# Performance work log

Measured on AMD Instinct MI355X. Metric: run time of the kernel, lower is better.

Reference implementation:

```python
import jax, jax.numpy as jnp
import numpy as np
from jax import lax

KERNEL = 3
NUM_ITER = 40
SMOOTH = 1.0


def _max_pool3d(x):
    # stride-1, SAME-padded 3x3x3 max pool over (B, C, D, H, W)
    return lax.reduce_window(x, -jnp.inf, lax.max,
                             (1, 1, KERNEL, KERNEL, KERNEL),
                             (1, 1, 1, 1, 1), 'SAME')


def _soft_erode(x):
    return -_max_pool3d(-x)


def _soft_open(x):
    return _max_pool3d(_soft_erode(x))


def soft_skel(img, num_iter=NUM_ITER):
    skel = jax.nn.relu(img - _soft_open(img))

    def body(carry, _):
        img, skel = carry
        img = _soft_erode(img)
        delta = jax.nn.relu(img - _soft_open(img))
        skel = skel + jax.nn.relu(delta - skel * delta)
        return (img, skel), None

    (_, skel), _ = lax.scan(body, (img, skel), None, length=num_iter)
    return skel


def reference(y_pred, y_true):
    p = jax.nn.sigmoid(y_pred)
    skel_pred = soft_skel(p)
    skel_true = soft_skel(y_true)
    tprec = (jnp.sum(skel_pred * y_true) + SMOOTH) / (jnp.sum(skel_pred) + SMOOTH)
    tsens = (jnp.sum(skel_true * p) + SMOOTH) / (jnp.sum(skel_true) + SMOOTH)
    cl_dice = 2.0 * (tprec * tsens) / (tprec + tsens + SMOOTH)
    return 1.0 - cl_dice


def setup_inputs() -> dict:
    key = jax.random.key(0)
    k1, k2 = jax.random.split(key)
    shape = (2, 1, 96, 256, 256)
    y_pred = jax.random.normal(k1, shape, dtype=jnp.float32)  # logits
    y_true = jax.random.uniform(k2, shape, dtype=jnp.float32)  # soft mask in [0,1]
    return {"y_pred": y_pred, "y_true": y_true}
```

## Files before the change

kernel.cpp:

```cpp
#include <hip/hip_runtime.h>
#include <hip/hip_fp16.h>
#include <math.h>

#define WW 256
#define HH 256
#define DDP 96
#define HWP (WW*HH)
#define DHW (DDP*HWP)
#define N2 (2*DHW)
#define N4 (4*DHW)
#define TX 128
#define TY 8
#define NT 256
#define ZS 12
#define NSLAB (DDP/ZS)
#define RED_BLOCKS 1024
#define NITER 40
#define RPAIRS 66
#define NSLOT ((TY+2)*RPAIRS)

typedef unsigned int u32;
typedef unsigned short u16;
typedef unsigned char u8;
typedef __half2 h2;

__device__ __forceinline__ float sigm(float x){return 1.f/(1.f+expf(-x));}
__device__ __forceinline__ int   icl(int v,int hi){return min(max(v,0),hi);}
__device__ __forceinline__ u32 h2u(h2 v){return __builtin_bit_cast(u32,v);}
__device__ __forceinline__ h2  u2h(u32 v){return __builtin_bit_cast(h2,v);}
__device__ __forceinline__ float2 up2(u32 v){return __half22float2(u2h(v));}
__device__ __forceinline__ u32 dn2(float a,float b){return h2u(__floats2half2_rn(a,b));}
__device__ __forceinline__ u32 pmin2(u32 a,u32 b){u32 d;asm("v_pk_min_f16 %0, %1, %2":"=v"(d):"v"(a),"v"(b));return d;}
__device__ __forceinline__ u32 pmax2(u32 a,u32 b){u32 d;asm("v_pk_max_f16 %0, %1, %2":"=v"(d):"v"(a),"v"(b));return d;}
__device__ __forceinline__ u32 psub2(u32 a,u32 b){u32 d;asm("v_pk_add_f16 %0, %1, %2 neg_lo:[0,1] neg_hi:[0,1]":"=v"(d):"v"(a),"v"(b));return d;}
__device__ __forceinline__ u32 pfma2(u32 a,u32 b,u32 c){u32 d;asm("v_pk_fma_f16 %0, %1, %2, %3":"=v"(d):"v"(a),"v"(b),"v"(c));return d;}
__device__ __forceinline__ u32 shpair(u32 hiSrc,u32 loSrc){return __builtin_amdgcn_alignbit(hiSrc,loSrc,16);}
__device__ __forceinline__ u32 sfix(u32 v,int m){
    if (m == 1) v = (v & 0xffffu) | (v << 16);
    else if (m == 2) v = (v >> 16) | (v & 0xffff0000u);
    return v;
}
__device__ __forceinline__ u32 pkrtz(float a,float b){
    return __builtin_bit_cast(u32, __builtin_amdgcn_cvt_pkrtz(a,b));
}
#define INF2P 0x7C007C00u
#define INF2N 0xFC00FC00u
#define C255_2 0x5BF85BF8u

__device__ __forceinline__ u32 pack_u8_sr(float s0,float s1,float s2,float s3,u32 h){
    float t0 = (float)( h        & 0xff);
    float t1 = (float)((h >>  8) & 0xff);
    float t2 = (float)((h >> 16) & 0xff);
    float t3 = (float)((h >> 24) & 0xff);
    int q0 = min((int)(s0*255.f + (t0+0.5f)*(1.f/256.f)), 255);
    int q1 = min((int)(s1*255.f + (t1+0.5f)*(1.f/256.f)), 255);
    int q2 = min((int)(s2*255.f + (t2+0.5f)*(1.f/256.f)), 255);
    int q3 = min((int)(s3*255.f + (t3+0.5f)*(1.f/256.f)), 255);
    return (u32)q0 | ((u32)q1<<8) | ((u32)q2<<16) | ((u32)q3<<24);
}

template<int MODE>
__global__ __launch_bounds__(NT) void step_kernel(const u16* __restrict__ ghalo,
                                                  u16* __restrict__ eaw,
                                                  const float* __restrict__ ypred,
                                                  const float* __restrict__ ytrue,
                                                  u8* __restrict__ skel,
                                                  int itno) {
    const int tx = threadIdx.x & 31;
    const int ty = threadIdx.x >> 5;
    const int x0 = blockIdx.x * TX;
    const int y0 = blockIdx.y * TY;
    const int vol = blockIdx.z / NSLAB;
    const int z0 = (blockIdx.z % NSLAB) * ZS;
    const size_t base = (size_t)vol * DHW;
    const int gxc = x0 + 4*tx;
    const int gyc = y0 + ty;
    const size_t co = (size_t)gyc*WW + gxc;

    const float* fin = nullptr;
    bool dosig = false;
    if (MODE == 0 || MODE == 1) {
        if (vol < 2) { fin = ypred + base; dosig = true; }
        else         { fin = ytrue + (size_t)(vol-2)*DHW; }
    }

    __shared__ u32 raw[2][TY+2][RPAIRS];

    const bool s2v = threadIdx.x < (NSLOT - 2*NT);
    u32 lo0, lo1, lo2;
    int md0, md1, md2;
    size_t po0, po1, po2;
    {
        #define SLOTSETUP(K, LO, MD, PO) {                         \
            int idx = threadIdx.x + (K)*NT;                        \
            int r = idx / RPAIRS;                                  \
            int w = idx - r*RPAIRS;                                \
            int gy = icl(y0-1+r, HH-1);                            \
            int gx0 = x0 - 2 + 2*w;                                \
            int m = 0, gx = gx0;                                   \
            if (gx0 < 0) { m = 1; gx = 0; }                        \
            else if (gx0 >= WW) { m = 2; gx = WW-2; }              \
            LO = r*RPAIRS + w; MD = m;                             \
            PO = (size_t)gy*WW + gx; }
        SLOTSETUP(0, lo0, md0, po0)
        SLOTSETUP(1, lo1, md1, po1)
        if (s2v) { SLOTSETUP(2, lo2, md2, po2) } else { lo2 = 0; md2 = 0; po2 = 0; }
        #undef SLOTSETUP
    }
    const u16*   hp0 = nullptr; const u16* hp1 = nullptr; const u16* hp2 = nullptr;
    const float* fp0 = nullptr; const float* fp1 = nullptr; const float* fp2 = nullptr;
    if (MODE == 0) {
        fp0 = fin + po0 + (size_t)(z0-1)*HWP;
        fp1 = fin + po1 + (size_t)(z0-1)*HWP;
        fp2 = fin + po2 + (size_t)(z0-1)*HWP;
    } else {
        hp0 = ghalo + base + po0 + (size_t)(z0-1)*HWP;
        hp1 = ghalo + base + po1 + (size_t)(z0-1)*HWP;
        hp2 = ghalo + base + po2 + (size_t)(z0-1)*HWP;
    }

    if (z0 >= 1) {
        const int b = (z0-1) & 1;
        u32 v0, v1, v2 = 0;
        if (MODE == 0) {
            float2 f0 = *(const float2*)fp0; v0 = dn2(f0.x, f0.y);
            float2 f1 = *(const float2*)fp1; v1 = dn2(f1.x, f1.y);
            if (s2v) { float2 f2 = *(const float2*)fp2; v2 = dn2(f2.x, f2.y); }
        } else {
            v0 = *(const u32*)hp0;
            v1 = *(const u32*)hp1;
            if (s2v) v2 = *(const u32*)hp2;
        }
        (&raw[b][0][0])[lo0] = sfix(v0, md0);
        (&raw[b][0][0])[lo1] = sfix(v1, md1);
        if (s2v) (&raw[b][0][0])[lo2] = sfix(v2, md2);
    }
    __syncthreads();

    const int wl = 2*tx;
    u32 n00,n01,n02, n10,n11,n12;
    u32 m00,m01,m02, m10,m11,m12;
    n00=n01=n02=n10=n11=n12=INF2P;
    m00=m01=m02=m10=m11=m12=INF2N;

    uint2 cv_c = make_uint2(0,0), cv_n = make_uint2(0,0);
    u32 sv_c = 0, sv_n = 0;
    float4 fv_c = make_float4(0,0,0,0), fv_n = make_float4(0,0,0,0);

    for (int zi = z0-1; zi <= z0+ZS; ++zi) {
        if (MODE == 0) { fp0 += HWP; fp1 += HWP; fp2 += HWP; }
        else           { hp0 += HWP; hp1 += HWP; hp2 += HWP; }
        const bool stage_ok = (zi < z0+ZS) && ((unsigned)(zi+1) < DDP);

        u32 v0 = 0, v1 = 0, v2 = 0;
        if (stage_ok) {
            if (MODE == 0) {
                float2 f0 = *(const float2*)fp0; v0 = dn2(f0.x, f0.y);
                float2 f1 = *(const float2*)fp1; v1 = dn2(f1.x, f1.y);
                if (s2v) { float2 f2 = *(const float2*)fp2; v2 = dn2(f2.x, f2.y); }
            } else {
                v0 = *(const u32*)hp0;
                v1 = *(const u32*)hp1;
                if (s2v) v2 = *(const u32*)hp2;
            }
        }
        if (MODE != 0 && zi >= z0 && zi < z0+ZS) {
            size_t pidx = base + (size_t)zi*HWP + co;
            if (MODE == 1) {
                fv_n = *(const float4*)(fin + (size_t)zi*HWP + co);
            } else {
                cv_n = *(const uint2*)(eaw + pidx);
                sv_n = *(const u32*)(skel + pidx);
            }
        }

        u32 xn0=INF2P, xn1=INF2P, xm0=INF2N, xm1=INF2N;
        if ((unsigned)zi < DDP) {
            const int b = zi & 1;
            uint2 a0 = *(const uint2*)&raw[b][ty  ][wl];
            uint2 b0 = *(const uint2*)&raw[b][ty  ][wl+2];
            uint2 a1 = *(const uint2*)&raw[b][ty+1][wl];
            uint2 b1 = *(const uint2*)&raw[b][ty+1][wl+2];
            uint2 a2 = *(const uint2*)&raw[b][ty+2][wl];
            uint2 b2 = *(const uint2*)&raw[b][ty+2][wl+2];
            u32 vnL  = pmin2(a0.x, pmin2(a1.x, a2.x));
            u32 vnM0 = pmin2(a0.y, pmin2(a1.y, a2.y));
            u32 vnM1 = pmin2(b0.x, pmin2(b1.x, b2.x));
            u32 vnR  = pmin2(b0.y, pmin2(b1.y, b2.y));
            u32 lsn  = shpair(vnM0, vnL);
            u32 rsn  = shpair(vnM1, vnM0);
            u32 rs1n = shpair(vnR,  vnM1);
            xn0 = pmin2(vnM0, pmin2(lsn, rsn));
            xn1 = pmin2(vnM1, pmin2(rsn, rs1n));
            if (MODE != 0) {
                u32 vmL  = pmax2(a0.x, pmax2(a1.x, a2.x));
                u32 vmM0 = pmax2(a0.y, pmax2(a1.y, a2.y));
                u32 vmM1 = pmax2(b0.x, pmax2(b1.x, b2.x));
                u32 vmR  = pmax2(b0.y, pmax2(b1.y, b2.y));
                u32 lsm  = shpair(vmM0, vmL);
                u32 rsm  = shpair(vmM1, vmM0);
                u32 rs1m = shpair(vmR,  vmM1);
                xm0 = pmax2(vmM0, pmax2(lsm, rsm));
                xm1 = pmax2(vmM1, pmax2(rsm, rs1m));
            }
        }
        n00=n01; n01=n02; n02=xn0;  n10=n11; n11=n12; n12=xn1;
        if (MODE != 0) { m00=m01; m01=m02; m02=xm0;  m10=m11; m11=m12; m12=xm1; }

        if (zi >= z0+1) {
            const int zc = zi - 1;
            size_t idx = base + (size_t)zc*HWP + co;
            u32 e0 = pmin2(n00, pmin2(n01, n02));
            u32 e1 = pmin2(n10, pmin2(n11, n12));
            if (MODE == 0) {
                if (dosig) {
                    float2 f0 = up2(e0), f1 = up2(e1);
                    e0 = dn2(sigm(f0.x), sigm(f0.y));
                    e1 = dn2(sigm(f1.x), sigm(f1.y));
                }
                *(uint2*)(eaw + idx) = make_uint2(e0, e1);
            } else if (MODE == 1) {
                float2 mA = up2(pmax2(m00, pmax2(m01, m02)));
                float2 mB = up2(pmax2(m10, pmax2(m11, m12)));
                float av0=fv_c.x, av1=fv_c.y, av2=fv_c.z, av3=fv_c.w;
                if (dosig) { av0=sigm(av0); av1=sigm(av1); av2=sigm(av2); av3=sigm(av3); }
                float d0 = fmaxf(av0 - mA.x, 0.f);
                float d1 = fmaxf(av1 - mA.y, 0.f);
                float d2 = fmaxf(av2 - mB.x, 0.f);
                float d3 = fmaxf(av3 - mB.y, 0.f);
                u32 lin = (u32)(idx >> 2);
                u32 h = lin * 2654435761u + (u32)itno * 0x9E3779B9u;
                *(u32*)(skel + idx) = pack_u8_sr(d0, d1, d2, d3, h);
                *(uint2*)(eaw + idx) = make_uint2(e0, e1);
            } else {
                u32 M3p0 = pmax2(m00, pmax2(m01, m02));
                u32 M3p1 = pmax2(m10, pmax2(m11, m12));
                u32 d0p = pmax2(psub2(cv_c.x, M3p0), 0u);
                u32 d1p = pmax2(psub2(cv_c.y, M3p1), 0u);
                u32 Sp0 = pkrtz((float)( sv_c        & 0xff), (float)((sv_c >>  8) & 0xff));
                u32 Sp1 = pkrtz((float)((sv_c >> 16) & 0xff), (float)((sv_c >> 24) & 0xff));
                u32 Sn0 = pfma2(d0p, psub2(C255_2, Sp0), Sp0);
                u32 Sn1 = pfma2(d1p, psub2(C255_2, Sp1), Sp1);
                float2 f0 = up2(Sn0), f1 = up2(Sn1);
                u32 lin = (u32)(idx >> 2);
                u32 h = lin * 2654435761u + (u32)itno * 0x9E3779B9u;
                u32 q0 = (u32)(f0.x + ((float)( h        & 0xff) + 0.5f)*(1.f/256.f));
                u32 q1 = (u32)(f0.y + ((float)((h >>  8) & 0xff) + 0.5f)*(1.f/256.f));
                u32 q2 = (u32)(f1.x + ((float)((h >> 16) & 0xff) + 0.5f)*(1.f/256.f));
                u32 q3 = (u32)(f1.y + ((float)((h >> 24) & 0xff) + 0.5f)*(1.f/256.f));
                *(u32*)(skel + idx) = q0 | (q1<<8) | (q2<<16) | (q3<<24);
                if (MODE != 3) *(uint2*)(eaw + idx) = make_uint2(e0, e1);
            }
        }
        cv_c = cv_n; sv_c = sv_n; fv_c = fv_n;

        if (stage_ok) {
            const int b = (zi+1) & 1;
            (&raw[b][0][0])[lo0] = sfix(v0, md0);
            (&raw[b][0][0])[lo1] = sfix(v1, md1);
            if (s2v) (&raw[b][0][0])[lo2] = sfix(v2, md2);
        }
        __syncthreads();
    }
}

__global__ __launch_bounds__(256) void reduce4_kernel(const u8* __restrict__ skel,
                                                      const float* __restrict__ ytrue,
                                                      const float* __restrict__ ypred,
                                                      float* __restrict__ part) {
    const u32* sp = (const u32*)skel;
    const u32* st = (const u32*)(skel + N2);
    const float4* yt = (const float4*)ytrue;
    const float4* yp = (const float4*)ypred;
    float a0=0.f,a1=0.f,a2=0.f,a3=0.f;
    for (int i = blockIdx.x*256 + threadIdx.x; i < N2/4; i += gridDim.x*256) {
        u32 a = sp[i]; u32 b = st[i];
        float4 t = yt[i]; float4 q = yp[i];
        float s0 = (float)( a        & 0xff) * (1.f/255.f);
        float s1 = (float)((a >>  8) & 0xff) * (1.f/255.f);
        float s2 = (float)((a >> 16) & 0xff) * (1.f/255.f);
        float s3 = (float)((a >> 24) & 0xff) * (1.f/255.f);
        float u0 = (float)( b        & 0xff) * (1.f/255.f);
        float u1 = (float)((b >>  8) & 0xff) * (1.f/255.f);
        float u2v= (float)((b >> 16) & 0xff) * (1.f/255.f);
        float u3 = (float)((b >> 24) & 0xff) * (1.f/255.f);
        a0 += s0*t.x + s1*t.y + s2*t.z + s3*t.w;
        a1 += s0 + s1 + s2 + s3;
        a2 += u0*sigm(q.x) + u1*sigm(q.y) + u2v*sigm(q.z) + u3*sigm(q.w);
        a3 += u0 + u1 + u2v + u3;
    }
    for (int off=32; off>0; off>>=1) {
        a0+=__shfl_down(a0,off); a1+=__shfl_down(a1,off);
        a2+=__shfl_down(a2,off); a3+=__shfl_down(a3,off);
    }
    __shared__ float red[4][4];
    int wave = threadIdx.x>>6;
    if ((threadIdx.x&63)==0){red[wave][0]=a0;red[wave][1]=a1;red[wave][2]=a2;red[wave][3]=a3;}
    __syncthreads();
    if (threadIdx.x==0){
        float s0=0,s1=0,s2=0,s3=0;
        for(int w=0;w<4;++w){s0+=red[w][0];s1+=red[w][1];s2+=red[w][2];s3+=red[w][3];}
        part[0*RED_BLOCKS+blockIdx.x]=s0; part[1*RED_BLOCKS+blockIdx.x]=s1;
        part[2*RED_BLOCKS+blockIdx.x]=s2; part[3*RED_BLOCKS+blockIdx.x]=s3;
    }
}

__global__ __launch_bounds__(256) void finalize_kernel(const float* __restrict__ part,
                                                       float* __restrict__ out) {
    float a0=0.f,a1=0.f,a2=0.f,a3=0.f;
    for (int i=threadIdx.x;i<RED_BLOCKS;i+=256){
        a0+=part[0*RED_BLOCKS+i]; a1+=part[1*RED_BLOCKS+i];
        a2+=part[2*RED_BLOCKS+i]; a3+=part[3*RED_BLOCKS+i];
    }
    for (int off=32; off>0; off>>=1){
        a0+=__shfl_down(a0,off); a1+=__shfl_down(a1,off);
        a2+=__shfl_down(a2,off); a3+=__shfl_down(a3,off);
    }
    __shared__ float red[4][4];
    int wave = threadIdx.x>>6;
    if ((threadIdx.x&63)==0){red[wave][0]=a0;red[wave][1]=a1;red[wave][2]=a2;red[wave][3]=a3;}
    __syncthreads();
    if (threadIdx.x==0){
        float s0=0,s1=0,s2=0,s3=0;
        for(int w=0;w<4;++w){s0+=red[w][0];s1+=red[w][1];s2+=red[w][2];s3+=red[w][3];}
        float tprec=(s0+1.f)/(s1+1.f);
        float tsens=(s2+1.f)/(s3+1.f);
        float cl2=2.f*tprec*tsens/(tprec+tsens+1.f);
        out[0]=1.f-cl2;
    }
}

__global__ void sentinel_kernel(float* out, float v){ out[0]=v; }

extern "C" void kernel_launch(void* const* d_in, const int* in_sizes, int n_in,
                              void* d_out, int out_size, void* d_ws, size_t ws_size,
                              hipStream_t stream) {
    const float* ypred = (const float*)d_in[0];
    const float* ytrue = (const float*)d_in[1];
    float* out = (float*)d_out;

    const size_t need = (size_t)2*N4*sizeof(u16) + (size_t)N4 + (size_t)4*RED_BLOCKS*sizeof(float);
    if (ws_size < need) { sentinel_kernel<<<1,1,0,stream>>>(out,-111111.f); return; }

    u16* EA   = (u16*)d_ws;
    u16* EB   = EA + N4;
    u8*  SKEL = (u8*)(EB + N4);
    float* PART = (float*)(SKEL + N4);

    dim3 grid(WW/TX, HH/TY, 4*NSLAB);

    step_kernel<0><<<grid, NT, 0, stream>>>(nullptr, EB, ypred, ytrue, nullptr, 0);
    step_kernel<1><<<grid, NT, 0, stream>>>(EB, EA, ypred, ytrue, SKEL, 0);

    u16* h = EA;
    u16* a = EB;
    for (int t = 1; t <= NITER; ++t) {
        if (t < NITER) step_kernel<2><<<grid, NT, 0, stream>>>(h, a, nullptr, nullptr, SKEL, t);
        else           step_kernel<3><<<grid, NT, 0, stream>>>(h, a, nullptr, nullptr, SKEL, t);
        u16* tmp = h; h = a; a = tmp;
    }

    reduce4_kernel<<<RED_BLOCKS, 256, 0, stream>>>(SKEL, ytrue, ypred, PART);
    finalize_kernel<<<1, 256, 0, stream>>>(PART, out);
}
```

Before: 1.669 ms.

## Prefetch halo planes two ahead and swizzle block order across XCDs

Halo loads for each z-plane are now issued two iterations ahead, with the shared-memory ring grown from two to four buffers, so global load latency overlaps more of the compute. The 3D grid becomes a 1D grid of 2048 blocks with a swizzle that maps consecutive block IDs to strided tiles, likely to spread neighbouring tiles across the chiplets or improve cache locality. The cost is more live registers and double the LDS per block, which could reduce occupancy.

```diff
diff --git a/kernel.cpp b/kernel.cpp
--- a/kernel.cpp
+++ b/kernel.cpp
@@ -18,6 +18,7 @@
 #define NITER 40
 #define RPAIRS 66
 #define NSLOT ((TY+2)*RPAIRS)
+#define NBLK 2048
 
 typedef unsigned int u32;
 typedef unsigned short u16;
@@ -66,12 +67,18 @@
                                                   const float* __restrict__ ytrue,
                                                   u8* __restrict__ skel,
                                                   int itno) {
+    const int bid = blockIdx.x;
+    const int swz = (bid & 7) * (NBLK/8) + (bid >> 3);
+    const int bx  = swz & 1;
+    const int by  = (swz >> 1) & 31;
+    const int bz  = swz >> 6;
+    const int vol = bz >> 3;
+    const int z0  = (bz & 7) * ZS;
+
     const int tx = threadIdx.x & 31;
     const int ty = threadIdx.x >> 5;
-    const int x0 = blockIdx.x * TX;
-    const int y0 = blockIdx.y * TY;
-    const int vol = blockIdx.z / NSLAB;
-    const int z0 = (blockIdx.z % NSLAB) * ZS;
+    const int x0 = bx * TX;
+    const int y0 = by * TY;
     const size_t base = (size_t)vol * DHW;
     const int gxc = x0 + 4*tx;
     const int gyc = y0 + ty;
@@ -84,7 +91,7 @@
         else         { fin = ytrue + (size_t)(vol-2)*DHW; }
     }
 
-    __shared__ u32 raw[2][TY+2][RPAIRS];
+    __shared__ u32 raw[4][TY+2][RPAIRS];
 
     const bool s2v = threadIdx.x < (NSLOT - 2*NT);
     u32 lo0, lo1, lo2;
@@ -107,33 +114,35 @@
         if (s2v) { SLOTSETUP(2, lo2, md2, po2) } else { lo2 = 0; md2 = 0; po2 = 0; }
         #undef SLOTSETUP
     }
-    const u16*   hp0 = nullptr; const u16* hp1 = nullptr; const u16* hp2 = nullptr;
-    const float* fp0 = nullptr; const float* fp1 = nullptr; const float* fp2 = nullptr;
-    if (MODE == 0) {
-        fp0 = fin + po0 + (size_t)(z0-1)*HWP;
-        fp1 = fin + po1 + (size_t)(z0-1)*HWP;
-        fp2 = fin + po2 + (size_t)(z0-1)*HWP;
+
+    const u16* hq0 = nullptr; const u16* hq1 = nullptr; const u16* hq2 = nullptr;
+    const float* fq0 = nullptr; const float* fq1 = nullptr; const float* fq2 = nullptr;
+    if (MODE == 0) { fq0 = fin + po0; fq1 = fin + po1; fq2 = fin + po2; }
+    else { hq0 = ghalo + base + po0; hq1 = ghalo + base + po1; hq2 = ghalo + base + po2; }
+
+    #define LOADP(Z, V0, V1, V2) {                                           \
+        if (MODE == 0) {                                                     \
+            float2 f0 = *(const float2*)(fq0 + (size_t)(Z)*HWP); V0 = dn2(f0.x,f0.y); \
+            float2 f1 = *(const float2*)(fq1 + (size_t)(Z)*HWP); V1 = dn2(f1.x,f1.y); \
+            if (s2v) { float2 f2 = *(const float2*)(fq2 + (size_t)(Z)*HWP); V2 = dn2(f2.x,f2.y); } \
+        } else {                                                             \
+            V0 = *(const u32*)(hq0 + (size_t)(Z)*HWP);                       \
+            V1 = *(const u32*)(hq1 + (size_t)(Z)*HWP);                       \
+            if (s2v) V2 = *(const u32*)(hq2 + (size_t)(Z)*HWP);              \
+        } }
+    #define WRITEP(B, V0, V1, V2) {                                          \
+        (&raw[B][0][0])[lo0] = sfix(V0, md0);                                \
+        (&raw[B][0][0])[lo1] = sfix(V1, md1);                                \
+        if (s2v) (&raw[B][0][0])[lo2] = sfix(V2, md2); }
+
+    u32 vN0 = 0, vN1 = 0, vN2 = 0;
+    if (z0 >= 1) {
+        u32 t0 = 0, t1 = 0, t2 = 0;
+        LOADP(z0-1, t0, t1, t2)
+        LOADP(z0, vN0, vN1, vN2)
+        WRITEP((z0-1)&3, t0, t1, t2)
     } else {
-        hp0 = ghalo + base + po0 + (size_t)(z0-1)*HWP;
-        hp1 = ghalo + base + po1 + (size_t)(z0-1)*HWP;
-        hp2 = ghalo + base + po2 + (size_t)(z0-1)*HWP;
-    }
-
-    if (z0 >= 1) {
-        const int b = (z0-1) & 1;
-        u32 v0, v1, v2 = 0;
-        if (MODE == 0) {
-            float2 f0 = *(const float2*)fp0; v0 = dn2(f0.x, f0.y);
-            float2 f1 = *(const float2*)fp1; v1 = dn2(f1.x, f1.y);
-            if (s2v) { float2 f2 = *(const float2*)fp2; v2 = dn2(f2.x, f2.y); }
-        } else {
-            v0 = *(const u32*)hp0;
-            v1 = *(const u32*)hp1;
-            if (s2v) v2 = *(const u32*)hp2;
-        }
-        (&raw[b][0][0])[lo0] = sfix(v0, md0);
-        (&raw[b][0][0])[lo1] = sfix(v1, md1);
-        if (s2v) (&raw[b][0][0])[lo2] = sfix(v2, md2);
+        LOADP(z0, vN0, vN1, vN2)
     }
     __syncthreads();
 
@@ -148,22 +157,10 @@
     float4 fv_c = make_float4(0,0,0,0), fv_n = make_float4(0,0,0,0);
 
     for (int zi = z0-1; zi <= z0+ZS; ++zi) {
-        if (MODE == 0) { fp0 += HWP; fp1 += HWP; fp2 += HWP; }
-        else           { hp0 += HWP; hp1 += HWP; hp2 += HWP; }
-        const bool stage_ok = (zi < z0+ZS) && ((unsigned)(zi+1) < DDP);
-
-        u32 v0 = 0, v1 = 0, v2 = 0;
-        if (stage_ok) {
-            if (MODE == 0) {
-                float2 f0 = *(const float2*)fp0; v0 = dn2(f0.x, f0.y);
-                float2 f1 = *(const float2*)fp1; v1 = dn2(f1.x, f1.y);
-                if (s2v) { float2 f2 = *(const float2*)fp2; v2 = dn2(f2.x, f2.y); }
-            } else {
-                v0 = *(const u32*)hp0;
-                v1 = *(const u32*)hp1;
-                if (s2v) v2 = *(const u32*)hp2;
-            }
-        }
+        const bool far_ok = (zi+2 <= z0+ZS) && (zi+2 < DDP);
+        u32 vF0 = 0, vF1 = 0, vF2 = 0;
+        if (far_ok) { LOADP(zi+2, vF0, vF1, vF2) }
+
         if (MODE != 0 && zi >= z0 && zi < z0+ZS) {
             size_t pidx = base + (size_t)zi*HWP + co;
             if (MODE == 1) {
@@ -176,7 +173,7 @@
 
         u32 xn0=INF2P, xn1=INF2P, xm0=INF2N, xm1=INF2N;
         if ((unsigned)zi < DDP) {
-            const int b = zi & 1;
+            const int b = zi & 3;
             uint2 a0 = *(const uint2*)&raw[b][ty  ][wl];
             uint2 b0 = *(const uint2*)&raw[b][ty  ][wl+2];
             uint2 a1 = *(const uint2*)&raw[b][ty+1][wl];
@@ -254,14 +251,13 @@
         }
         cv_c = cv_n; sv_c = sv_n; fv_c = fv_n;
 
-        if (stage_ok) {
-            const int b = (zi+1) & 1;
-            (&raw[b][0][0])[lo0] = sfix(v0, md0);
-            (&raw[b][0][0])[lo1] = sfix(v1, md1);
-            if (s2v) (&raw[b][0][0])[lo2] = sfix(v2, md2);
-        }
+        const bool near_ok = (zi+1 <= z0+ZS) && (zi+1 < DDP);
+        if (near_ok) { WRITEP((zi+1)&3, vN0, vN1, vN2) }
+        vN0 = vF0; vN1 = vF1; vN2 = vF2;
         __syncthreads();
     }
+    #undef LOADP
+    #undef WRITEP
 }
 
 __global__ __launch_bounds__(256) void reduce4_kernel(const u8* __restrict__ skel,
@@ -347,16 +343,14 @@
     u8*  SKEL = (u8*)(EB + N4);
     float* PART = (float*)(SKEL + N4);
 
-    dim3 grid(WW/TX, HH/TY, 4*NSLAB);
-
-    step_kernel<0><<<grid, NT, 0, stream>>>(nullptr, EB, ypred, ytrue, nullptr, 0);
-    step_kernel<1><<<grid, NT, 0, stream>>>(EB, EA, ypred, ytrue, SKEL, 0);
+    step_kernel<0><<<NBLK, NT, 0, stream>>>(nullptr, EB, ypred, ytrue, nullptr, 0);
+    step_kernel<1><<<NBLK, NT, 0, stream>>>(EB, EA, ypred, ytrue, SKEL, 0);
 
     u16* h = EA;
     u16* a = EB;
     for (int t = 1; t <= NITER; ++t) {
-        if (t < NITER) step_kernel<2><<<grid, NT, 0, stream>>>(h, a, nullptr, nullptr, SKEL, t);
-        else           step_kernel<3><<<grid, NT, 0, stream>>>(h, a, nullptr, nullptr, SKEL, t);
+        if (t < NITER) step_kernel<2><<<NBLK, NT, 0, stream>>>(h, a, nullptr, nullptr, SKEL, t);
+        else           step_kernel<3><<<NBLK, NT, 0, stream>>>(h, a, nullptr, nullptr, SKEL, t);
         u16* tmp = h; h = a; a = tmp;
     }
 
```

Measured after the change: 1.416 ms. 15.1% less time.
